# Performance work log

Measured on AMD Instinct MI355X. Metric: run time of the kernel, lower is better.

Reference implementation:

```python
import jax, jax.numpy as jnp
import numpy as np

N_NODES = 100000


def gcn_conv(x, edge_index, W, b, n_nodes):
    # PyG GCNConv: x' = D^{-1/2} (A + I) D^{-1/2} (x W) + b
    src, dst = edge_index[0], edge_index[1]
    h = x @ W  # linear transform first (in_ch >= out_ch path in PyG)
    # degree with self-loops, computed on target nodes
    deg = jax.ops.segment_sum(jnp.ones_like(dst, dtype=h.dtype), dst,
                              num_segments=n_nodes) + 1.0
    dinv = jax.lax.rsqrt(deg)  # deg >= 1 due to self-loops
    # edge messages: norm_e * h[src]
    norm_e = dinv[src] * dinv[dst]  # [E]
    msg = h[src] * norm_e[:, None]  # [E, out]
    agg = jax.ops.segment_sum(msg, dst, num_segments=n_nodes)
    # self-loop contribution: dinv[i]^2 * h[i]
    out = agg + h * (dinv * dinv)[:, None] + b
    return out


def setup_inputs() -> dict:
    key = jax.random.key(0)
    k1, k2, k3, k4 = jax.random.split(key, 4)
    N, E, F, H, C = N_NODES, 1600000, 128, 64, 32
    x = jax.random.normal(k1, (N, F), dtype=jnp.float32)
    edge_index = jax.random.randint(k2, (2, E), 0, N, dtype=jnp.int64)
    # glorot-style init
    W1 = jax.random.normal(k3, (F, H), dtype=jnp.float32) * (1.0 / np.sqrt(F))
    W2 = jax.random.normal(k4, (H, C), dtype=jnp.float32) * (1.0 / np.sqrt(H))
    b1 = jnp.zeros((H,), dtype=jnp.float32)
    b2 = jnp.zeros((C,), dtype=jnp.float32)
    return {"x": x, "edge_index": edge_index, "W1": W1, "b1": b1,
            "W2": W2, "b2": b2}


def reference(x, edge_index, W1, b1, W2, b2):
    n = x.shape[0]
    h = gcn_conv(x, edge_index, W1, b1, n)
    h = jax.nn.relu(h)
    # dropout is identity in eval mode (reference baseline)
    out = gcn_conv(h, edge_index, W2, b2, n)
    return out
```

## Files before the change

kernel.cpp:

```cpp
#include <hip/hip_runtime.h>
#include <hip/hip_fp16.h>

#define B_HIST 512
#define SHIFT  9

typedef _Float16 f16x8 __attribute__((ext_vector_type(8)));
typedef float f32x4 __attribute__((ext_vector_type(4)));


__global__ __launch_bounds__(256) void p1_hist(const int* __restrict__ dst,
                                               int* __restrict__ histT, int E) {
  __shared__ int h[256];
  const int t = threadIdx.x;
  h[t] = 0;
  __syncthreads();
  const int epb = (E + B_HIST - 1) / B_HIST;
  const int beg = blockIdx.x * epb;
  const int end = min(beg + epb, E);
  for (int e = beg + t; e < end; e += 256)
    atomicAdd(&h[dst[e] >> SHIFT], 1);
  __syncthreads();
  histT[t * B_HIST + blockIdx.x] = h[t];
}

__global__ __launch_bounds__(256) void p2a_colscan(int* __restrict__ histT,
                                                   int* __restrict__ bsum) {
  __shared__ int sdata[256];
  const int bin = blockIdx.x, t = threadIdx.x;
  const int i0 = bin * B_HIST + 2 * t;
  int c0 = histT[i0], c1 = histT[i0 + 1];
  int s = c0 + c1;
  sdata[t] = s;
  __syncthreads();
  for (int off = 1; off < 256; off <<= 1) {
    int x = 0;
    if (t >= off) x = sdata[t - off];
    __syncthreads();
    if (t >= off) sdata[t] += x;
    __syncthreads();
  }
  int excl = sdata[t] - s;
  histT[i0] = excl;
  histT[i0 + 1] = excl + c0;
  if (t == 255) bsum[bin] = sdata[255];
}

__global__ __launch_bounds__(256) void p2b_scan(const int* __restrict__ bsum,
                                                int* __restrict__ colstart) {
  __shared__ int sdata[256];
  const int t = threadIdx.x;
  int v = bsum[t];
  sdata[t] = v;
  __syncthreads();
  for (int off = 1; off < 256; off <<= 1) {
    int x = 0;
    if (t >= off) x = sdata[t - off];
    __syncthreads();
    if (t >= off) sdata[t] += x;
    __syncthreads();
  }
  colstart[t] = sdata[t] - v;
  if (t == 255) colstart[256] = sdata[255];
}

__global__ __launch_bounds__(256) void p3_scatter(const int* __restrict__ src,
                                                  const int* __restrict__ dst,
                                                  const int* __restrict__ histT,
                                                  const int* __restrict__ colstart,
                                                  int* __restrict__ pbuf, int E) {
  __shared__ int cur[256];
  const int t = threadIdx.x;
  cur[t] = colstart[t] + histT[t * B_HIST + blockIdx.x];
  __syncthreads();
  const int epb = (E + B_HIST - 1) / B_HIST;
  const int beg = blockIdx.x * epb;
  const int end = min(beg + epb, E);
  for (int e = beg + t; e < end; e += 256) {
    int d = dst[e];
    int s = src[e];
    int pos = atomicAdd(&cur[d >> SHIFT], 1);
    pbuf[pos] = ((d & 511) << 17) | s;
  }
}

__global__ __launch_bounds__(256) void p4_fine(const int* __restrict__ pbuf,
                                               const int* __restrict__ colstart,
                                               int* __restrict__ rowptr,
                                               float* __restrict__ dinv,
                                               int* __restrict__ ssrc, int N, int NB) {
  __shared__ int cnt[512];
  __shared__ int sdata[256];
  __shared__ int cur[512];
  const int b = blockIdx.x, t = threadIdx.x;
  const int base = colstart[b], endp = colstart[b + 1];
  cnt[2 * t] = 0; cnt[2 * t + 1] = 0;
  __syncthreads();
  for (int i = base + t; i < endp; i += 256)
    atomicAdd(&cnt[pbuf[i] >> 17], 1);
  __syncthreads();
  int c0 = cnt[2 * t], c1 = cnt[2 * t + 1];
  int s = c0 + c1;
  sdata[t] = s;
  __syncthreads();
  for (int off = 1; off < 256; off <<= 1) {
    int x = 0;
    if (t >= off) x = sdata[t - off];
    __syncthreads();
    if (t >= off) sdata[t] += x;
    __syncthreads();
  }
  int excl = sdata[t] - s;
  int e0 = base + excl, e1 = base + excl + c0;
  cur[2 * t] = e0;
  cur[2 * t + 1] = e1;
  int node0 = (b << SHIFT) + 2 * t;
  if (node0 < N) {
    rowptr[node0] = e0;
    dinv[node0] = rsqrtf((float)c0 + 1.0f);
  }
  if (node0 + 1 < N) {
    rowptr[node0 + 1] = e1;
    dinv[node0 + 1] = rsqrtf((float)c1 + 1.0f);
  }
  if (b == NB - 1 && t == 0) rowptr[N] = endp;
  __syncthreads();
  for (int i = base + t; i < endp; i += 256) {
    int p = pbuf[i];
    int pos = atomicAdd(&cur[p >> 17], 1);
    ssrc[pos] = p & 0x1FFFF;
  }
}


template <int COLS, int K>
__global__ __launch_bounds__(256) void mfma_gemm(const float* __restrict__ X,
                                                 const float* __restrict__ W,
                                                 const float* __restrict__ dinv,
                                                 __half* __restrict__ O, int N) {
  constexpr int NKK = K / 32;
  constexpr int NCT = COLS / 16;
  constexpr int RCH = K / 8;
  constexpr int SWM = RCH - 1;
  __shared__ _Float16 xs[64 * K];
  __shared__ _Float16 wb[K * COLS];
  const int t = threadIdx.x;
  const int row0 = blockIdx.x * 64;

  for (int task = t; task < NKK * 4 * COLS; task += 256) {
    int col = task % COLS;
    int kq = task / COLS;
    _Float16 tmp[8];
#pragma unroll
    for (int j = 0; j < 8; ++j)
      tmp[j] = (_Float16)W[(kq * 8 + j) * COLS + col];
    *reinterpret_cast<f16x8*>(&wb[task * 8]) = *reinterpret_cast<const f16x8*>(tmp);
  }
  for (int task = t; task < 64 * RCH; task += 256) {
    int row = task / RCH, c = task % RCH;
    int grow = row0 + row;
    float4 v0 = make_float4(0.f, 0.f, 0.f, 0.f), v1 = v0;
    if (grow < N) {
      const float4* xr = reinterpret_cast<const float4*>(X + (size_t)grow * K);
      v0 = xr[c * 2];
      v1 = xr[c * 2 + 1];
    }
    _Float16 tmp[8] = {(_Float16)v0.x, (_Float16)v0.y, (_Float16)v0.z, (_Float16)v0.w,
                       (_Float16)v1.x, (_Float16)v1.y, (_Float16)v1.z, (_Float16)v1.w};
    int sc = c ^ (row & SWM);
    *reinterpret_cast<f16x8*>(&xs[row * K + sc * 8]) = *reinterpret_cast<const f16x8*>(tmp);
  }
  __syncthreads();

  const int wave = t >> 6, lane = t & 63;
  const int q = lane >> 4, c = lane & 15;
  const int wrow = wave * 16;

  f16x8 bfrag[NKK][NCT];
#pragma unroll
  for (int kk = 0; kk < NKK; ++kk)
#pragma unroll
    for (int ct = 0; ct < NCT; ++ct)
      bfrag[kk][ct] = *reinterpret_cast<const f16x8*>(
          &wb[(size_t)((kk * 4 + q) * COLS + ct * 16 + c) * 8]);

  f32x4 acc[NCT];
#pragma unroll
  for (int ct = 0; ct < NCT; ++ct) acc[ct] = {0.f, 0.f, 0.f, 0.f};

#pragma unroll
  for (int kk = 0; kk < NKK; ++kk) {
    int row = wrow + c;
    int cc = (kk * 4 + q) ^ (row & SWM);
    f16x8 afrag = *reinterpret_cast<const f16x8*>(&xs[row * K + cc * 8]);
#pragma unroll
    for (int ct = 0; ct < NCT; ++ct)
      acc[ct] = __builtin_amdgcn_mfma_f32_16x16x32_f16(afrag, bfrag[kk][ct], acc[ct], 0, 0, 0);
  }

#pragma unroll
  for (int r = 0; r < 4; ++r) {
    int row = row0 + wrow + q * 4 + r;
    if (row < N) {
      float di = dinv[row];
#pragma unroll
      for (int ct = 0; ct < NCT; ++ct)
        O[(size_t)row * COLS + ct * 16 + c] = __float2half(acc[ct][r] * di);
    }
  }
}


__global__ __launch_bounds__(256) void gather64_kernel(const int* __restrict__ rowptr,
                                                       const int* __restrict__ ssrc,
                                                       const float* __restrict__ dinv,
                                                       const uint2* __restrict__ g,
                                                       const float4* __restrict__ bias,
                                                       float4* __restrict__ outb, int N) {
  int node = (blockIdx.x * 256 + threadIdx.x) >> 4;
  int col = threadIdx.x & 15;
  if (node >= N) return;
  int beg = rowptr[node], end = rowptr[node + 1];
  float4 a0 = {0.f, 0.f, 0.f, 0.f}, a1 = a0;
  for (int i = beg; i < end; i += 8) {
    int cnt = end - i;
    uint2 v[8];
#pragma unroll
    for (int u = 0; u < 8; ++u) {
      if (u < cnt) {
        int s = ssrc[i + u];
        v[u] = g[(size_t)s * 16 + col];
      }
    }
#pragma unroll
    for (int u = 0; u < 8; ++u) {
      if (u < cnt) {
        float2 f0 = __half22float2(*(__half2*)&v[u].x);
        float2 f1 = __half22float2(*(__half2*)&v[u].y);
        if (u & 1) { a1.x += f0.x; a1.y += f0.y; a1.z += f1.x; a1.w += f1.y; }
        else       { a0.x += f0.x; a0.y += f0.y; a0.z += f1.x; a0.w += f1.y; }
      }
    }
  }
  uint2 vs = g[(size_t)node * 16 + col];
  float2 g01 = __half22float2(*(__half2*)&vs.x);
  float2 g23 = __half22float2(*(__half2*)&vs.y);
  float di = dinv[node];
  float4 bb = bias[col];
  float4 o;
  o.x = fmaxf(fmaf(di, (a0.x + a1.x) + g01.x, bb.x), 0.f);
  o.y = fmaxf(fmaf(di, (a0.y + a1.y) + g01.y, bb.y), 0.f);
  o.z = fmaxf(fmaf(di, (a0.z + a1.z) + g23.x, bb.z), 0.f);
  o.w = fmaxf(fmaf(di, (a0.w + a1.w) + g23.y, bb.w), 0.f);
  outb[(size_t)node * 16 + col] = o;
}

__global__ __launch_bounds__(256) void gather32_kernel(const int* __restrict__ rowptr,
                                                       const int* __restrict__ ssrc,
                                                       const float* __restrict__ dinv,
                                                       const uint2* __restrict__ g,
                                                       const float4* __restrict__ bias,
                                                       float4* __restrict__ outb, int N) {
  int node = (blockIdx.x * 256 + threadIdx.x) >> 3;
  int col = threadIdx.x & 7;
  if (node >= N) return;
  int beg = rowptr[node], end = rowptr[node + 1];
  float4 a0 = {0.f, 0.f, 0.f, 0.f}, a1 = a0;
  for (int i = beg; i < end; i += 8) {
    int cnt = end - i;
    uint2 v[8];
#pragma unroll
    for (int u = 0; u < 8; ++u) {
      if (u < cnt) {
        int s = ssrc[i + u];
        v[u] = g[(size_t)s * 8 + col];
      }
    }
#pragma unroll
    for (int u = 0; u < 8; ++u) {
      if (u < cnt) {
        float2 f0 = __half22float2(*(__half2*)&v[u].x);
        float2 f1 = __half22float2(*(__half2*)&v[u].y);
        if (u & 1) { a1.x += f0.x; a1.y += f0.y; a1.z += f1.x; a1.w += f1.y; }
        else       { a0.x += f0.x; a0.y += f0.y; a0.z += f1.x; a0.w += f1.y; }
      }
    }
  }
  uint2 vs = g[(size_t)node * 8 + col];
  float2 g01 = __half22float2(*(__half2*)&vs.x);
  float2 g23 = __half22float2(*(__half2*)&vs.y);
  float di = dinv[node];
  float4 bb = bias[col];
  float4 o;
  o.x = fmaf(di, (a0.x + a1.x) + g01.x, bb.x);
  o.y = fmaf(di, (a0.y + a1.y) + g01.y, bb.y);
  o.z = fmaf(di, (a0.z + a1.z) + g23.x, bb.z);
  o.w = fmaf(di, (a0.w + a1.w) + g23.y, bb.w);
  outb[(size_t)node * 8 + col] = o;
}


extern "C" void kernel_launch(void* const* d_in, const int* in_sizes, int n_in,
                              void* d_out, int out_size, void* d_ws, size_t ws_size,
                              hipStream_t stream) {
  const float* x  = (const float*)d_in[0];
  const int*   ei = (const int*)d_in[1];
  const float* W1 = (const float*)d_in[2];
  const float* b1 = (const float*)d_in[3];
  const float* W2 = (const float*)d_in[4];
  const float* b2 = (const float*)d_in[5];
  float* out = (float*)d_out;

  const int H = in_sizes[3];
  const int F = in_sizes[2] / H;
  const int N = in_sizes[0] / F;
  const int E = in_sizes[1] / 2;
  const int* src = ei;
  const int* dst = ei + E;
  const int NB = (N + 511) >> SHIFT;

  char* w = (char*)d_ws;
  auto alloc = [&](size_t bytes) { char* p = w; w += (bytes + 255) & ~(size_t)255; return p; };
  int*    histT    = (int*)alloc((size_t)256 * B_HIST * 4);
  int*    bsum     = (int*)alloc(256 * 4);
  int*    colstart = (int*)alloc(257 * 4);
  int*    pbuf     = (int*)alloc((size_t)E * 4);
  int*    ssrc     = (int*)alloc((size_t)E * 4);
  int*    rowptr   = (int*)alloc((size_t)(N + 1) * 4);
  float*  dinv     = (float*)alloc((size_t)N * 4);
  __half* g1       = (__half*)alloc((size_t)N * 64 * 2);
  float*  buf1     = (float*)alloc((size_t)N * 64 * 4);
  __half* g2       = (__half*)alloc((size_t)N * 32 * 2);

  p1_hist<<<B_HIST, 256, 0, stream>>>(dst, histT, E);
  p2a_colscan<<<256, 256, 0, stream>>>(histT, bsum);
  p2b_scan<<<1, 256, 0, stream>>>(bsum, colstart);
  p3_scatter<<<B_HIST, 256, 0, stream>>>(src, dst, histT, colstart, pbuf, E);
  p4_fine<<<NB, 256, 0, stream>>>(pbuf, colstart, rowptr, dinv, ssrc, N, NB);

  mfma_gemm<64, 128><<<(N + 63) / 64, 256, 0, stream>>>(x, W1, dinv, g1, N);
  gather64_kernel<<<(N * 16 + 255) / 256, 256, 0, stream>>>(rowptr, ssrc, dinv,
      (const uint2*)g1, (const float4*)b1, (float4*)buf1, N);

  mfma_gemm<32, 64><<<(N + 63) / 64, 256, 0, stream>>>(buf1, W2, dinv, g2, N);
  gather32_kernel<<<(N * 8 + 255) / 256, 256, 0, stream>>>(rowptr, ssrc, dinv,
      (const uint2*)g2, (const float4*)b2, (float4*)out, N);
}
```

Measured before the change: 144.8 us.

## Split gather into 16-column slices with column-sliced GEMM output layout

The GEMM now writes its fp16 output in column-slice-major layout (one [N,16] slab per 16 columns). Each aggregation layer runs as several launches, each gathering one 16-column slice with 4 threads per node. Each slab is N*16*2 bytes (about 3.2 MB), so the random-access gather working set per pass is much smaller and more likely to stay in L2. The cost is rereading rowptr and ssrc once per slice and paying more kernel launches.

```diff
diff --git a/kernel.cpp b/kernel.cpp
--- a/kernel.cpp
+++ b/kernel.cpp
@@ -204,20 +204,22 @@
       float di = dinv[row];
 #pragma unroll
       for (int ct = 0; ct < NCT; ++ct)
-        O[(size_t)row * COLS + ct * 16 + c] = __float2half(acc[ct][r] * di);
+        O[((size_t)ct * N + row) * 16 + c] = __float2half(acc[ct][r] * di);
     }
   }
 }
 
 
-__global__ __launch_bounds__(256) void gather64_kernel(const int* __restrict__ rowptr,
-                                                       const int* __restrict__ ssrc,
-                                                       const float* __restrict__ dinv,
-                                                       const uint2* __restrict__ g,
-                                                       const float4* __restrict__ bias,
-                                                       float4* __restrict__ outb, int N) {
-  int node = (blockIdx.x * 256 + threadIdx.x) >> 4;
-  int col = threadIdx.x & 15;
+template <bool RELU>
+__global__ __launch_bounds__(256) void gatherS_kernel(const int* __restrict__ rowptr,
+                                                      const int* __restrict__ ssrc,
+                                                      const float* __restrict__ dinv,
+                                                      const uint2* __restrict__ gq,
+                                                      const float* __restrict__ biasq,
+                                                      float* __restrict__ outb,
+                                                      int ldo, int N) {
+  int node = (blockIdx.x * 256 + threadIdx.x) >> 2;
+  int col4 = threadIdx.x & 3;
   if (node >= N) return;
   int beg = rowptr[node], end = rowptr[node + 1];
   float4 a0 = {0.f, 0.f, 0.f, 0.f}, a1 = a0;
@@ -228,7 +230,7 @@
     for (int u = 0; u < 8; ++u) {
       if (u < cnt) {
         int s = ssrc[i + u];
-        v[u] = g[(size_t)s * 16 + col];
+        v[u] = gq[(size_t)s * 4 + col4];
       }
     }
 #pragma unroll
@@ -241,61 +243,21 @@
       }
     }
   }
-  uint2 vs = g[(size_t)node * 16 + col];
+  uint2 vs = gq[(size_t)node * 4 + col4];
   float2 g01 = __half22float2(*(__half2*)&vs.x);
   float2 g23 = __half22float2(*(__half2*)&vs.y);
   float di = dinv[node];
-  float4 bb = bias[col];
-  float4 o;
-  o.x = fmaxf(fmaf(di, (a0.x + a1.x) + g01.x, bb.x), 0.f);
-  o.y = fmaxf(fmaf(di, (a0.y + a1.y) + g01.y, bb.y), 0.f);
-  o.z = fmaxf(fmaf(di, (a0.z + a1.z) + g23.x, bb.z), 0.f);
-  o.w = fmaxf(fmaf(di, (a0.w + a1.w) + g23.y, bb.w), 0.f);
-  outb[(size_t)node * 16 + col] = o;
-}
-
-__global__ __launch_bounds__(256) void gather32_kernel(const int* __restrict__ rowptr,
-                                                       const int* __restrict__ ssrc,
-                                                       const float* __restrict__ dinv,
-                                                       const uint2* __restrict__ g,
-                                                       const float4* __restrict__ bias,
-                                                       float4* __restrict__ outb, int N) {
-  int node = (blockIdx.x * 256 + threadIdx.x) >> 3;
-  int col = threadIdx.x & 7;
-  if (node >= N) return;
-  int beg = rowptr[node], end = rowptr[node + 1];
-  float4 a0 = {0.f, 0.f, 0.f, 0.f}, a1 = a0;
-  for (int i = beg; i < end; i += 8) {
-    int cnt = end - i;
-    uint2 v[8];
-#pragma unroll
-    for (int u = 0; u < 8; ++u) {
-      if (u < cnt) {
-        int s = ssrc[i + u];
-        v[u] = g[(size_t)s * 8 + col];
-      }
-    }
-#pragma unroll
-    for (int u = 0; u < 8; ++u) {
-      if (u < cnt) {
-        float2 f0 = __half22float2(*(__half2*)&v[u].x);
-        float2 f1 = __half22float2(*(__half2*)&v[u].y);
-        if (u & 1) { a1.x += f0.x; a1.y += f0.y; a1.z += f1.x; a1.w += f1.y; }
-        else       { a0.x += f0.x; a0.y += f0.y; a0.z += f1.x; a0.w += f1.y; }
-      }
-    }
-  }
-  uint2 vs = g[(size_t)node * 8 + col];
-  float2 g01 = __half22float2(*(__half2*)&vs.x);
-  float2 g23 = __half22float2(*(__half2*)&vs.y);
-  float di = dinv[node];
-  float4 bb = bias[col];
+  float4 bb = reinterpret_cast<const float4*>(biasq)[col4];
   float4 o;
   o.x = fmaf(di, (a0.x + a1.x) + g01.x, bb.x);
   o.y = fmaf(di, (a0.y + a1.y) + g01.y, bb.y);
   o.z = fmaf(di, (a0.z + a1.z) + g23.x, bb.z);
   o.w = fmaf(di, (a0.w + a1.w) + g23.y, bb.w);
-  outb[(size_t)node * 8 + col] = o;
+  if (RELU) {
+    o.x = fmaxf(o.x, 0.f); o.y = fmaxf(o.y, 0.f);
+    o.z = fmaxf(o.z, 0.f); o.w = fmaxf(o.w, 0.f);
+  }
+  reinterpret_cast<float4*>(outb + (size_t)node * ldo)[col4] = o;
 }
 
 
@@ -337,11 +299,15 @@
   p3_scatter<<<B_HIST, 256, 0, stream>>>(src, dst, histT, colstart, pbuf, E);
   p4_fine<<<NB, 256, 0, stream>>>(pbuf, colstart, rowptr, dinv, ssrc, N, NB);
 
+  const int gblocks = (N * 4 + 255) / 256;
+
   mfma_gemm<64, 128><<<(N + 63) / 64, 256, 0, stream>>>(x, W1, dinv, g1, N);
-  gather64_kernel<<<(N * 16 + 255) / 256, 256, 0, stream>>>(rowptr, ssrc, dinv,
-      (const uint2*)g1, (const float4*)b1, (float4*)buf1, N);
+  for (int q = 0; q < 4; ++q)
+    gatherS_kernel<true><<<gblocks, 256, 0, stream>>>(rowptr, ssrc, dinv,
+        (const uint2*)(g1 + (size_t)q * N * 16), b1 + q * 16, buf1 + q * 16, 64, N);
 
   mfma_gemm<32, 64><<<(N + 63) / 64, 256, 0, stream>>>(buf1, W2, dinv, g2, N);
-  gather32_kernel<<<(N * 8 + 255) / 256, 256, 0, stream>>>(rowptr, ssrc, dinv,
-      (const uint2*)g2, (const float4*)b2, (float4*)out, N);
-}
+  for (int q = 0; q < 2; ++q)
+    gatherS_kernel<false><<<gblocks, 256, 0, stream>>>(rowptr, ssrc, dinv,
+        (const uint2*)(g2 + (size_t)q * N * 16), b2 + q * 16, out + q * 16, 32, N);
+}
```

New measurement: 191.8 us. 1.32x slower.
